# Performance work log

Hardware: AMD Instinct MI355X
Metric: run time of the kernel (lower is better)

The kernel has to match this reference:

```python
import jax, jax.numpy as jnp
import numpy as np


def _pos_enc(seq_len, d_model, dtype):
    # PositionalEncoding2D buffer: interleaved sin/cos, standard transformer PE
    pos = jnp.arange(seq_len, dtype=dtype)[:, None]                      # [S,1]
    div = jnp.exp(jnp.arange(0, d_model, 2, dtype=dtype) * (-(np.log(10000.0) / d_model)))  # [d/2]
    pe = jnp.zeros((seq_len, d_model), dtype=dtype)
    pe = pe.at[:, 0::2].set(jnp.sin(pos * div))
    pe = pe.at[:, 1::2].set(jnp.cos(pos * div))
    return pe


def setup_inputs() -> dict:
    key = jax.random.key(0)
    k1, k2 = jax.random.split(key)
    B, C, H, W = 32, 384, 32, 32
    d = C
    x = jax.random.normal(k1, (B, C, H, W), dtype=jnp.float32)
    # fused QKV projection weight (stored as [d, 3d] so y = x @ W + b)
    Wqkv = jax.random.normal(k2, (d, 3 * d), dtype=jnp.float32) * (1.0 / np.sqrt(d))
    b = jnp.zeros((3 * d,), dtype=jnp.float32)
    return {"x": x, "W": Wqkv, "b": b}


def reference(x, W, b):
    B, C, H, Wd = x.shape
    d = C
    S = H * Wd
    xs = x.reshape(B, C, S).transpose(0, 2, 1)          # [B,S,d]
    xs = xs + _pos_enc(S, d, xs.dtype)                  # add positional encoding
    qkv = xs @ W + b                                    # [B,S,3d]
    q, k, v = jnp.split(qkv, 3, axis=-1)                # each [B,S,d]
    scores = jnp.einsum('bqd,bkd->bqk', q, k) / (d ** 0.5)  # [B,S,S]
    attn = jax.nn.softmax(scores, axis=-1)
    weighted = jnp.einsum('bqk,bkd->bqd', attn, v)      # [B,S,d]
    return weighted.transpose(0, 2, 1).reshape(B, C, H, Wd)
```

## Files before the change

### kernel.cpp

```cpp
#include <hip/hip_runtime.h>
#include <hip/hip_bf16.h>
#include <math.h>

typedef __attribute__((ext_vector_type(8))) __bf16 bf16x8;
typedef __attribute__((ext_vector_type(4))) float f32x4;

#define S_LEN 1024
#define D_MODEL 384
#define BATCH 32
#define N3 1152
#define KVB 32
#define NT (S_LEN / KVB)

#define MFMA16(a, b, c) __builtin_amdgcn_mfma_f32_16x16x32_bf16((a), (b), (c), 0, 0, 0)

static __device__ __forceinline__ ushort f2bf(float f) {
    __bf16 h = (__bf16)f;
    return __builtin_bit_cast(ushort, h);
}
static __device__ __forceinline__ uint pk2(float a, float b) {
    return (uint)f2bf(a) | ((uint)f2bf(b) << 16);
}

__global__ void pe_kernel(float* peT) {
    int idx = blockIdx.x * 256 + threadIdx.x;
    int k = idx >> 10, s = idx & 1023;
    float e = -(float)((k >> 1) * 2) * (logf(10000.0f) / (float)D_MODEL);
    float div = expf(e);
    float a = (float)s * div;
    peT[idx] = (k & 1) ? cosf(a) : sinf(a);
}

__global__ void wt_kernel(const float* __restrict__ W, ushort* __restrict__ Wt) {
    __shared__ float tile[32][33];
    int n0 = blockIdx.x * 32, k0 = blockIdx.y * 32;
    int tx = threadIdx.x, ty = threadIdx.y;
#pragma unroll
    for (int r = 0; r < 4; ++r) {
        int kl = ty * 4 + r;
        tile[kl][tx] = W[(size_t)(k0 + kl) * N3 + n0 + tx];
    }
    __syncthreads();
#pragma unroll
    for (int r = 0; r < 4; ++r) {
        int nl = ty * 4 + r;
        Wt[(size_t)(n0 + nl) * D_MODEL + k0 + tx] = f2bf(tile[tx][nl]);
    }
}

__global__ void astage_kernel(const float* __restrict__ x, const float* __restrict__ peT,
                              ushort* __restrict__ A) {
    __shared__ float tile[32][33];
    int s0 = blockIdx.x * 32, k0 = blockIdx.y * 32, b = blockIdx.z;
    int tx = threadIdx.x, ty = threadIdx.y;
#pragma unroll
    for (int r = 0; r < 4; ++r) {
        int kl = ty * 4 + r;
        tile[kl][tx] = x[(size_t)(b * D_MODEL + k0 + kl) * S_LEN + s0 + tx]
                     + peT[(size_t)(k0 + kl) * S_LEN + s0 + tx];
    }
    __syncthreads();
#pragma unroll
    for (int r = 0; r < 4; ++r) {
        int sl = ty * 4 + r;
        A[(size_t)(b * S_LEN + s0 + sl) * D_MODEL + k0 + tx] = f2bf(tile[tx][sl]);
    }
}

__global__ __launch_bounds__(256) void qkv_gemm(const ushort* __restrict__ A,
                                                const ushort* __restrict__ Wt,
                                                const float* __restrict__ bias,
                                                ushort* __restrict__ qkv,
                                                ushort* __restrict__ Vt) {
    __shared__ __align__(16) ushort As[128 * 32];
    __shared__ __align__(16) ushort Bs[128 * 32];
    int id = blockIdx.x;
    int g = id / 288, loc = id % 288;
    int nt_ = loc / 32, mt_ = g * 32 + (loc % 32);
    int m0 = mt_ * 128, n0 = nt_ * 128;
    int tid = threadIdx.x;
    int wave = tid >> 6, lane = tid & 63;
    int i16 = lane & 15, gq = lane >> 4;
    int wr = wave >> 1, wc = wave & 1;
    f32x4 acc[4][4] = {};
    for (int ks = 0; ks < 12; ++ks) {
        int k0 = ks * 32;
        __syncthreads();
#pragma unroll
        for (int i = 0; i < 2; ++i) {
            int off = (wave * 2 + i) * 1024;
            int row = (off >> 6) + (lane >> 2);
            int kc = lane & 3;
            const ushort* ga = A + (size_t)(m0 + row) * D_MODEL + k0 + kc * 8;
            __builtin_amdgcn_global_load_lds(
                (const __attribute__((address_space(1))) uint32_t*)ga,
                (__attribute__((address_space(3))) uint32_t*)((char*)As + off), 16, 0, 0);
            const ushort* gb = Wt + (size_t)(n0 + row) * D_MODEL + k0 + kc * 8;
            __builtin_amdgcn_global_load_lds(
                (const __attribute__((address_space(1))) uint32_t*)gb,
                (__attribute__((address_space(3))) uint32_t*)((char*)Bs + off), 16, 0, 0);
        }
        __syncthreads();
        bf16x8 af[4], bfr[4];
#pragma unroll
        for (int mt = 0; mt < 4; ++mt) {
            int row = wr * 64 + mt * 16 + i16;
            af[mt] = *reinterpret_cast<const bf16x8*>(&As[row * 32 + gq * 8]);
        }
#pragma unroll
        for (int nt = 0; nt < 4; ++nt) {
            int row = wc * 64 + nt * 16 + i16;
            bfr[nt] = *reinterpret_cast<const bf16x8*>(&Bs[row * 32 + gq * 8]);
        }
#pragma unroll
        for (int mt = 0; mt < 4; ++mt)
#pragma unroll
            for (int nt = 0; nt < 4; ++nt)
                acc[mt][nt] = MFMA16(af[mt], bfr[nt], acc[mt][nt]);
    }
    if (n0 < 2 * D_MODEL) {
#pragma unroll
        for (int nt = 0; nt < 4; ++nt) {
            int n = n0 + wc * 64 + nt * 16 + i16;
            float bv = bias[n];
#pragma unroll
            for (int mt = 0; mt < 4; ++mt)
#pragma unroll
                for (int r = 0; r < 4; ++r) {
                    int m = m0 + wr * 64 + mt * 16 + gq * 4 + r;
                    qkv[(size_t)m * N3 + n] = f2bf(acc[mt][nt][r] + bv);
                }
        }
    } else {
        int b = m0 >> 10;
        int s_base = (m0 & 1023) + wr * 64;
#pragma unroll
        for (int nt = 0; nt < 4; ++nt) {
            int n = n0 + wc * 64 + nt * 16 + i16;
            float bv = bias[n];
            int c = n - 2 * D_MODEL;
            ushort* vrow = Vt + (size_t)(b * D_MODEL + c) * S_LEN;
#pragma unroll
            for (int mt = 0; mt < 4; ++mt) {
                int s = s_base + mt * 16 + gq * 4;
                ushort4 p4;
                p4.x = f2bf(acc[mt][nt][0] + bv);
                p4.y = f2bf(acc[mt][nt][1] + bv);
                p4.z = f2bf(acc[mt][nt][2] + bv);
                p4.w = f2bf(acc[mt][nt][3] + bv);
                *reinterpret_cast<ushort4*>(vrow + s) = p4;
            }
        }
    }
}

__global__ __launch_bounds__(256, 2) void attn_kernel(const ushort* __restrict__ qkv,
                                                      const ushort* __restrict__ Vt,
                                                      float* __restrict__ out) {
    __shared__ __align__(16) ushort Ks[12 * 32 * 32];
    __shared__ __align__(16) ushort Vts[384 * 32];
    __shared__ __align__(16) ushort Pq[2][32 * 32];
    __shared__ float Ltab[2][2][2][16];
    int id = blockIdx.x;
    int xcd = id & 7, slot = (id >> 3) & 3, qt = id >> 5;
    int b = slot * 8 + xcd;
    int tid = threadIdx.x;
    int wave = tid >> 6, lane = tid & 63;
    int i16 = lane & 15, gq = lane >> 4;
    int qg = wave & 1, h = wave >> 1;
    int q0w = qt * 64 + qg * 32;

    const ushort* Kbase = qkv + (size_t)b * S_LEN * N3 + D_MODEL;
    const ushort* Vbase = Vt + (size_t)b * D_MODEL * S_LEN;

    auto stage_K = [&](int kv0) {
#pragma unroll
        for (int r = 0; r < 6; ++r) {
            int ii = wave * 6 + r;
            int kt = ii >> 1, jb = (ii & 1) * 16;
            int j = jb + (lane >> 2), ck = lane & 3;
            const ushort* ga = Kbase + (size_t)(kv0 + j) * N3 + kt * 32 + ck * 8;
            __builtin_amdgcn_global_load_lds(
                (const __attribute__((address_space(1))) uint32_t*)ga,
                (__attribute__((address_space(3))) uint32_t*)((char*)Ks + ii * 1024), 16, 0, 0);
        }
    };
    auto stage_V = [&](int kv0) {
#pragma unroll
        for (int r = 0; r < 6; ++r) {
            int ii = wave * 6 + r;
            int c = ii * 16 + (lane >> 2), ck = lane & 3;
            const ushort* ga = Vbase + (size_t)c * S_LEN + kv0 + ck * 8;
            __builtin_amdgcn_global_load_lds(
                (const __attribute__((address_space(1))) uint32_t*)ga,
                (__attribute__((address_space(3))) uint32_t*)((char*)Vts + ii * 1024), 16, 0, 0);
        }
    };

    stage_K(0);
    stage_V(0);

    bf16x8 qf[12][2];
    const ushort* Qb0 = qkv + (size_t)(b * S_LEN + q0w + i16) * N3;
    const ushort* Qb1 = qkv + (size_t)(b * S_LEN + q0w + 16 + i16) * N3;
#pragma unroll
    for (int kt = 0; kt < 12; ++kt) {
        qf[kt][0] = *reinterpret_cast<const bf16x8*>(Qb0 + kt * 32 + gq * 8);
        qf[kt][1] = *reinterpret_cast<const bf16x8*>(Qb1 + kt * 32 + gq * 8);
    }

    f32x4 oc[12][2] = {};
    float lsum0 = 0.f, lsum1 = 0.f;
    const float sl2e = 0.05103103630798287f * 1.4426950408889634f;

    char* PqB = (char*)&Pq[qg][0];

    for (int t = 0; t < NT; ++t) {
        asm volatile("s_waitcnt vmcnt(0)" ::: "memory");
        __builtin_amdgcn_s_barrier();
        __builtin_amdgcn_sched_barrier(0);

        const char* Kb = (const char*)Ks;
        f32x4 sacc0 = {}, sacc1 = {};
        __builtin_amdgcn_s_setprio(1);
#pragma unroll
        for (int kt = 0; kt < 12; ++kt) {
            bf16x8 kf = *reinterpret_cast<const bf16x8*>(
                Kb + kt * 2048 + (h * 16 + i16) * 64 + gq * 16);
            sacc0 = MFMA16(kf, qf[kt][0], sacc0);
            sacc1 = MFMA16(kf, qf[kt][1], sacc1);
        }
        __builtin_amdgcn_s_setprio(0);

        float p00 = exp2f(sacc0[0] * sl2e), p01 = exp2f(sacc0[1] * sl2e);
        float p02 = exp2f(sacc0[2] * sl2e), p03 = exp2f(sacc0[3] * sl2e);
        float p10 = exp2f(sacc1[0] * sl2e), p11 = exp2f(sacc1[1] * sl2e);
        float p12 = exp2f(sacc1[2] * sl2e), p13 = exp2f(sacc1[3] * sl2e);
        lsum0 += (p00 + p01) + (p02 + p03);
        lsum1 += (p10 + p11) + (p12 + p13);
        {
            uint2 w0; w0.x = pk2(p00, p01); w0.y = pk2(p02, p03);
            uint2 w1; w1.x = pk2(p10, p11); w1.y = pk2(p12, p13);
            *reinterpret_cast<uint2*>(PqB + i16 * 64 + h * 32 + gq * 8) = w0;
            *reinterpret_cast<uint2*>(PqB + (16 + i16) * 64 + h * 32 + gq * 8) = w1;
        }
        asm volatile("s_waitcnt lgkmcnt(0)" ::: "memory");
        __builtin_amdgcn_s_barrier();
        __builtin_amdgcn_sched_barrier(0);
        if (t + 1 < NT) stage_K((t + 1) * KVB);

        bf16x8 pf0 = *reinterpret_cast<const bf16x8*>(PqB + i16 * 64 + gq * 16);
        bf16x8 pf1 = *reinterpret_cast<const bf16x8*>(PqB + (16 + i16) * 64 + gq * 16);
        const char* Vb = (const char*)Vts;
        __builtin_amdgcn_s_setprio(1);
#pragma unroll
        for (int ct = 0; ct < 12; ++ct) {
            bf16x8 vf = *reinterpret_cast<const bf16x8*>(
                Vb + (h * 12 + ct) * 1024 + i16 * 64 + gq * 16);
            oc[ct][0] = MFMA16(vf, pf0, oc[ct][0]);
            oc[ct][1] = MFMA16(vf, pf1, oc[ct][1]);
        }
        __builtin_amdgcn_s_setprio(0);
        __builtin_amdgcn_s_barrier();
        __builtin_amdgcn_sched_barrier(0);
        if (t + 1 < NT) stage_V((t + 1) * KVB);
    }

    lsum0 += __shfl_xor(lsum0, 16); lsum0 += __shfl_xor(lsum0, 32);
    lsum1 += __shfl_xor(lsum1, 16); lsum1 += __shfl_xor(lsum1, 32);
    __syncthreads();
    if (gq == 0) {
        Ltab[qg][h][0][i16] = lsum0;
        Ltab[qg][h][1][i16] = lsum1;
    }
    __syncthreads();
    float inv0 = 1.0f / (Ltab[qg][0][0][i16] + Ltab[qg][1][0][i16]);
    float inv1 = 1.0f / (Ltab[qg][0][1][i16] + Ltab[qg][1][1][i16]);

    float* obase = out + (size_t)b * D_MODEL * S_LEN + q0w + i16;
#pragma unroll
    for (int ct = 0; ct < 12; ++ct)
#pragma unroll
        for (int r = 0; r < 4; ++r) {
            int c = h * 192 + ct * 16 + gq * 4 + r;
            obase[(size_t)c * S_LEN] = oc[ct][0][r] * inv0;
            obase[(size_t)c * S_LEN + 16] = oc[ct][1][r] * inv1;
        }
}

extern "C" void kernel_launch(void* const* d_in, const int* in_sizes, int n_in,
                              void* d_out, int out_size, void* d_ws, size_t ws_size,
                              hipStream_t stream) {
    const float* x    = (const float*)d_in[0];
    const float* W    = (const float*)d_in[1];
    const float* bias = (const float*)d_in[2];
    float* out = (float*)d_out;

    char* ws = (char*)d_ws;
    ushort* A_bf  = (ushort*)(ws);
    ushort* Wt    = (ushort*)(ws + 25165824);
    float*  peT   = (float*)(ws + 26050560);
    ushort* qkv   = (ushort*)(ws + 27623424);
    ushort* Vt    = (ushort*)(ws + 103120896);

    pe_kernel<<<1536, 256, 0, stream>>>(peT);
    wt_kernel<<<dim3(36, 12), dim3(32, 8), 0, stream>>>(W, Wt);
    astage_kernel<<<dim3(32, 12, 32), dim3(32, 8), 0, stream>>>(x, peT, A_bf);
    qkv_gemm<<<2304, 256, 0, stream>>>(A_bf, Wt, bias, qkv, Vt);
    attn_kernel<<<512, 256, 0, stream>>>(qkv, Vt, out);
}
```

Baseline: 156.4 us.

## Double-buffer V tiles and relayout LDS to avoid bank conflicts

V tiles are now double-buffered in LDS so the next K and V tiles are issued together right after the P-write barrier, which removes the third barrier per iteration. K, V and P are stored in LDS as k-chunk-major with 16-byte rows instead of 64-byte rows, so the MFMA fragment reads stride cleanly and avoid bank conflicts. The wait counters are adjusted so only the K loads must have landed before the QK step. The cost is extra LDS for the second V buffer, which may affect the two-blocks-per-CU occupancy.

```diff
diff --git a/kernel.cpp b/kernel.cpp
--- a/kernel.cpp
+++ b/kernel.cpp
@@ -157,9 +157,9 @@
 __global__ __launch_bounds__(256, 2) void attn_kernel(const ushort* __restrict__ qkv,
                                                       const ushort* __restrict__ Vt,
                                                       float* __restrict__ out) {
-    __shared__ __align__(16) ushort Ks[12 * 32 * 32];
-    __shared__ __align__(16) ushort Vts[384 * 32];
-    __shared__ __align__(16) ushort Pq[2][32 * 32];
+    __shared__ __align__(16) ushort Ks[12 * 4 * 32 * 8];
+    __shared__ __align__(16) ushort Vts[2][24 * 4 * 16 * 8];
+    __shared__ __align__(16) ushort Pq[2][4 * 32 * 8];
     __shared__ float Ltab[2][2][2][16];
     int id = blockIdx.x;
     int xcd = id & 7, slot = (id >> 3) & 3, qt = id >> 5;
@@ -172,33 +172,33 @@
 
     const ushort* Kbase = qkv + (size_t)b * S_LEN * N3 + D_MODEL;
     const ushort* Vbase = Vt + (size_t)b * D_MODEL * S_LEN;
+    int l31 = lane & 31, l5 = lane >> 5;
+    int l15 = lane & 15, l4 = lane >> 4;
 
     auto stage_K = [&](int kv0) {
 #pragma unroll
         for (int r = 0; r < 6; ++r) {
             int ii = wave * 6 + r;
-            int kt = ii >> 1, jb = (ii & 1) * 16;
-            int j = jb + (lane >> 2), ck = lane & 3;
-            const ushort* ga = Kbase + (size_t)(kv0 + j) * N3 + kt * 32 + ck * 8;
+            int kt = ii >> 1, half = ii & 1;
+            const ushort* ga = Kbase + (size_t)(kv0 + l31) * N3 + kt * 32 + (half * 2 + l5) * 8;
             __builtin_amdgcn_global_load_lds(
                 (const __attribute__((address_space(1))) uint32_t*)ga,
                 (__attribute__((address_space(3))) uint32_t*)((char*)Ks + ii * 1024), 16, 0, 0);
         }
     };
-    auto stage_V = [&](int kv0) {
+    auto stage_V = [&](int kv0, int bi) {
 #pragma unroll
         for (int r = 0; r < 6; ++r) {
             int ii = wave * 6 + r;
-            int c = ii * 16 + (lane >> 2), ck = lane & 3;
-            const ushort* ga = Vbase + (size_t)c * S_LEN + kv0 + ck * 8;
+            const ushort* ga = Vbase + (size_t)(ii * 16 + l15) * S_LEN + kv0 + l4 * 8;
             __builtin_amdgcn_global_load_lds(
                 (const __attribute__((address_space(1))) uint32_t*)ga,
-                (__attribute__((address_space(3))) uint32_t*)((char*)Vts + ii * 1024), 16, 0, 0);
+                (__attribute__((address_space(3))) uint32_t*)((char*)&Vts[bi][0] + ii * 1024), 16, 0, 0);
         }
     };
 
     stage_K(0);
-    stage_V(0);
+    stage_V(0, 0);
 
     bf16x8 qf[12][2];
     const ushort* Qb0 = qkv + (size_t)(b * S_LEN + q0w + i16) * N3;
@@ -214,9 +214,11 @@
     const float sl2e = 0.05103103630798287f * 1.4426950408889634f;
 
     char* PqB = (char*)&Pq[qg][0];
+    const int kread = gq * 512 + (h * 16 + i16) * 16;
+    const int vread = gq * 256 + i16 * 16;
 
     for (int t = 0; t < NT; ++t) {
-        asm volatile("s_waitcnt vmcnt(0)" ::: "memory");
+        asm volatile("s_waitcnt vmcnt(6) lgkmcnt(0)" ::: "memory");
         __builtin_amdgcn_s_barrier();
         __builtin_amdgcn_sched_barrier(0);
 
@@ -225,8 +227,7 @@
         __builtin_amdgcn_s_setprio(1);
 #pragma unroll
         for (int kt = 0; kt < 12; ++kt) {
-            bf16x8 kf = *reinterpret_cast<const bf16x8*>(
-                Kb + kt * 2048 + (h * 16 + i16) * 64 + gq * 16);
+            bf16x8 kf = *reinterpret_cast<const bf16x8*>(Kb + kt * 2048 + kread);
             sacc0 = MFMA16(kf, qf[kt][0], sacc0);
             sacc1 = MFMA16(kf, qf[kt][1], sacc1);
         }
@@ -239,31 +240,31 @@
         lsum0 += (p00 + p01) + (p02 + p03);
         lsum1 += (p10 + p11) + (p12 + p13);
         {
+            int pw = (h * 2 + (gq >> 1)) * 512 + (gq & 1) * 8;
             uint2 w0; w0.x = pk2(p00, p01); w0.y = pk2(p02, p03);
             uint2 w1; w1.x = pk2(p10, p11); w1.y = pk2(p12, p13);
-            *reinterpret_cast<uint2*>(PqB + i16 * 64 + h * 32 + gq * 8) = w0;
-            *reinterpret_cast<uint2*>(PqB + (16 + i16) * 64 + h * 32 + gq * 8) = w1;
-        }
-        asm volatile("s_waitcnt lgkmcnt(0)" ::: "memory");
+            *reinterpret_cast<uint2*>(PqB + pw + i16 * 16) = w0;
+            *reinterpret_cast<uint2*>(PqB + pw + (16 + i16) * 16) = w1;
+        }
+        asm volatile("s_waitcnt vmcnt(0) lgkmcnt(0)" ::: "memory");
         __builtin_amdgcn_s_barrier();
         __builtin_amdgcn_sched_barrier(0);
-        if (t + 1 < NT) stage_K((t + 1) * KVB);
-
-        bf16x8 pf0 = *reinterpret_cast<const bf16x8*>(PqB + i16 * 64 + gq * 16);
-        bf16x8 pf1 = *reinterpret_cast<const bf16x8*>(PqB + (16 + i16) * 64 + gq * 16);
-        const char* Vb = (const char*)Vts;
+        if (t + 1 < NT) {
+            stage_K((t + 1) * KVB);
+            stage_V((t + 1) * KVB, (t + 1) & 1);
+        }
+
+        bf16x8 pf0 = *reinterpret_cast<const bf16x8*>(PqB + gq * 512 + i16 * 16);
+        bf16x8 pf1 = *reinterpret_cast<const bf16x8*>(PqB + gq * 512 + (16 + i16) * 16);
+        const char* Vb = (const char*)&Vts[t & 1][0];
         __builtin_amdgcn_s_setprio(1);
 #pragma unroll
         for (int ct = 0; ct < 12; ++ct) {
-            bf16x8 vf = *reinterpret_cast<const bf16x8*>(
-                Vb + (h * 12 + ct) * 1024 + i16 * 64 + gq * 16);
+            bf16x8 vf = *reinterpret_cast<const bf16x8*>(Vb + (h * 12 + ct) * 1024 + vread);
             oc[ct][0] = MFMA16(vf, pf0, oc[ct][0]);
             oc[ct][1] = MFMA16(vf, pf1, oc[ct][1]);
         }
         __builtin_amdgcn_s_setprio(0);
-        __builtin_amdgcn_s_barrier();
-        __builtin_amdgcn_sched_barrier(0);
-        if (t + 1 < NT) stage_V((t + 1) * KVB);
     }
 
     lsum0 += __shfl_xor(lsum0, 16); lsum0 += __shfl_xor(lsum0, 32);
```

Result: slower. 179.1 us (+14.5%).
